# Optimization experiments

Measured on AMD Instinct MI355X. Metric: run time of the kernel, lower is better.

The kernel has to match this reference:

```python
import jax, jax.numpy as jnp
import numpy as np
import math

V, E, H, NL = 10000, 256, 512, 2
B, T = 64, 128


def _lstm_cell(x, h, c, Wih, Whh, b):
    # PyTorch gate order: i, f, g, o
    gates = x @ Wih.T + h @ Whh.T + b
    i, f, g, o = jnp.split(gates, 4, axis=-1)
    c = jax.nn.sigmoid(f) * c + jax.nn.sigmoid(i) * jnp.tanh(g)
    h = jax.nn.sigmoid(o) * jnp.tanh(c)
    return h, c


def _run_layer(xs, Wih, Whh, b):
    # xs: [T, B, D]; returns outputs [T, B, H] and final (h, c)
    Bn = xs.shape[1]
    h0 = jnp.zeros((Bn, H), xs.dtype)
    c0 = jnp.zeros((Bn, H), xs.dtype)

    def step(carry, x):
        h, c = carry
        h, c = _lstm_cell(x, h, c, Wih, Whh, b)
        return (h, c), h

    (hT, cT), ys = jax.lax.scan(step, (h0, c0), xs)
    return ys, hT, cT


def setup_inputs() -> dict:
    key = jax.random.key(0)
    ks = jax.random.split(key, 24)
    s = 0.05

    def n(k, shape):
        return jax.random.normal(k, shape, dtype=jnp.float32) * s

    inp = {
        "input_ids": jax.random.randint(ks[0], (B, T), 0, V),
        "my_attention_mask": jax.random.randint(ks[1], (B, T), 0, 2),
        "update_step": 1000,
        # encoder params
        "enc_embed": n(ks[2], (V, E)),
        "enc_Wih0": n(ks[3], (4 * H, E)),
        "enc_Whh0": n(ks[4], (4 * H, H)),
        "enc_b0": n(ks[5], (4 * H,)),
        "enc_Wih1": n(ks[6], (4 * H, H)),
        "enc_Whh1": n(ks[7], (4 * H, H)),
        "enc_b1": n(ks[8], (4 * H,)),
        # decoder params
        "dec_embed": n(ks[9], (V, E)),
        "dec_Wih0": n(ks[10], (4 * H, E)),
        "dec_Whh0": n(ks[11], (4 * H, H)),
        "dec_b0": n(ks[12], (4 * H,)),
        "dec_Wih1": n(ks[13], (4 * H, H)),
        "dec_Whh1": n(ks[14], (4 * H, H)),
        "dec_b1": n(ks[15], (4 * H,)),
        "dec_Wout": n(ks[16], (V, H)),
        "dec_bout": n(ks[17], (V,)),
    }
    return inp


def _forward(input_ids, my_attention_mask, update_step,
             enc_embed, enc_Wih0, enc_Whh0, enc_b0, enc_Wih1, enc_Whh1, enc_b1,
             dec_embed, dec_Wih0, dec_Whh0, dec_b0, dec_Wih1, dec_Whh1, dec_b1,
             dec_Wout, dec_bout):
    temp_ids = input_ids.T                      # [T, B]
    mask = my_attention_mask                    # [B, T]

    # ---- encoder: 2-layer LSTM over the full sequence ----
    emb = enc_embed[temp_ids]                   # [T, B, E]
    ys0, h0, c0 = _run_layer(emb, enc_Wih0, enc_Whh0, enc_b0)
    _, h1, c1 = _run_layer(ys0, enc_Wih1, enc_Whh1, enc_b1)

    def dec_step(carry, tok):
        dh0, dc0, dh1, dc1 = carry
        x = dec_embed[tok]                      # [B, E]
        dh0, dc0 = _lstm_cell(x, dh0, dc0, dec_Wih0, dec_Whh0, dec_b0)
        dh1, dc1 = _lstm_cell(dh0, dh1, dc1, dec_Wih1, dec_Whh1, dec_b1)
        out = dh1 @ dec_Wout.T + dec_bout       # [B, V]
        return (dh0, dc0, dh1, dc1), out

    _, dec_outs = jax.lax.scan(dec_step, (h0, c0, h1, c1), temp_ids[:-1])  # [T-1, B, V]

    # ---- mask-driven compaction: outputs[i, j] = dec_out at t where
    #      i = exclusive-cumsum of mask[j, :t]; unwritten slots stay random ----
    outputs = jax.random.uniform(jax.random.key(42), (T, B, V), dtype=jnp.float32)
    idx = jnp.cumsum(mask, axis=1) - mask       # exclusive cumsum, [B, T]
    write_i = jnp.where(mask[:, 1:] > 0, idx[:, 1:], T)   # OOB -> dropped
    vals = jnp.transpose(dec_outs, (1, 0, 2))   # [B, T-1, V]
    outputs = outputs.at[write_i, jnp.arange(B)[:, None]].set(vals, mode="drop")

    # ---- hard gumbel-softmax with straight-through ----
    temperature = max(0.5, math.exp(-0.003 * update_step))
    eps = 1e-20
    U = jax.random.uniform(jax.random.key(7), (T, B, V), dtype=jnp.float32)
    g = -jnp.log(-jnp.log(U + eps) + eps)
    y = jax.nn.softmax((outputs + g) / temperature, axis=-1)
    y_hard = jax.nn.one_hot(jnp.argmax(y, axis=-1), V, dtype=y.dtype)
    gs = jax.lax.stop_gradient(y_hard - y) + y  # [T, B, V]

    # ---- scatter back into padded layout: masked positions pull compacted
    #      gumbel onehots, unmasked positions get onehot(input id) ----
    gathered = gs[jnp.clip(idx, 0, T - 1), jnp.arange(B)[:, None]]  # [B, T, V]
    id_onehot = jax.nn.one_hot(input_ids, V, dtype=jnp.float32)     # [B, T, V]
    onehots = jnp.where((mask > 0)[:, :, None], gathered, id_onehot)
    return onehots.reshape(B * T, V)


def reference(input_ids, my_attention_mask, update_step,
              enc_embed, enc_Wih0, enc_Whh0, enc_b0, enc_Wih1, enc_Whh1, enc_b1,
              dec_embed, dec_Wih0, dec_Whh0, dec_b0, dec_Wih1, dec_Whh1, dec_b1,
              dec_Wout, dec_bout):
    return _forward(input_ids, my_attention_mask, update_step,
                    enc_embed, enc_Wih0, enc_Whh0, enc_b0, enc_Wih1, enc_Whh1, enc_b1,
                    dec_embed, dec_Wih0, dec_Whh0, dec_b0, dec_Wih1, dec_Whh1, dec_b1,
                    dec_Wout, dec_bout)
```

## Files before the change

kernel.cpp:

```cpp
#include <hip/hip_runtime.h>
#include <stdint.h>


typedef short bf16x8 __attribute__((ext_vector_type(8)));
typedef float f32x4 __attribute__((ext_vector_type(4)));

__device__ __forceinline__ void threefry2x32(uint32_t k0, uint32_t k1,
                                             uint32_t x0, uint32_t x1,
                                             uint32_t& o0, uint32_t& o1)
{
  const uint32_t k2 = k0 ^ k1 ^ 0x1BD11BDAu;
  x0 += k0; x1 += k1;
#define TF_R(r) x0 += x1; x1 = (x1 << r) | (x1 >> (32 - r)); x1 ^= x0;
  TF_R(13) TF_R(15) TF_R(26) TF_R(6)
  x0 += k1; x1 += k2 + 1u;
  TF_R(17) TF_R(29) TF_R(16) TF_R(24)
  x0 += k2; x1 += k0 + 2u;
  TF_R(13) TF_R(15) TF_R(26) TF_R(6)
  x0 += k0; x1 += k1 + 3u;
  TF_R(17) TF_R(29) TF_R(16) TF_R(24)
  x0 += k1; x1 += k2 + 4u;
  TF_R(13) TF_R(15) TF_R(26) TF_R(6)
  x0 += k2; x1 += k0 + 5u;
#undef TF_R
  o0 = x0; o1 = x1;
}

__device__ __forceinline__ float jax_uniform(uint32_t seed, uint32_t i)
{
  uint32_t o0, o1;
  threefry2x32(0u, seed, 0u, i, o0, o1);
  const uint32_t bits = o0 ^ o1;
  return __uint_as_float(0x3F800000u | (bits >> 9)) - 1.0f;
}

__device__ __forceinline__ ushort f2bf(float x)
{
  const uint32_t u = __float_as_uint(x);
  const uint32_t r = u + 0x7FFFu + ((u >> 16) & 1u);
  return (ushort)(r >> 16);
}
__device__ __forceinline__ float bf2f(ushort b)
{
  return __uint_as_float(((uint32_t)b) << 16);
}

__device__ __forceinline__ unsigned long long packkey(float f, int n)
{
  uint32_t u = __float_as_uint(f);
  u = (u & 0x80000000u) ? ~u : (u | 0x80000000u);
  return ((unsigned long long)u << 32) | (uint32_t)(0x7FFFFFFF - n);
}

__global__ __launch_bounds__(256)
void split_kernel(const float* __restrict__ src, ushort* __restrict__ hi,
                  ushort* __restrict__ lo, int n)
{
  const int i = blockIdx.x * 256 + threadIdx.x;
  if (i < n) {
    const float v = src[i];
    const ushort h = f2bf(v);
    hi[i] = h;
    lo[i] = f2bf(v - bf2f(h));
  }
}

__global__ __launch_bounds__(256)
void transpose_split_kernel(const float* __restrict__ seq,
                            ushort* __restrict__ Thi, ushort* __restrict__ Tlo)
{
  __shared__ float tile[128][65];
  const int t = blockIdx.x >> 2;
  const int kc = blockIdx.x & 3;
  const int tid = threadIdx.x;
  const float* sbase = seq + (size_t)t * 32768 + (size_t)kc * 128 * 64;
#pragma unroll
  for (int it = 0; it < 32; ++it) {
    const int idx = it * 256 + tid;
    tile[idx >> 6][idx & 63] = sbase[idx];
  }
  __syncthreads();
#pragma unroll
  for (int it = 0; it < 32; ++it) {
    const int idx = it * 256 + tid;
    const int b = idx >> 7, k = idx & 127;
    const float v = tile[k][b];
    const size_t o = ((size_t)t * 64 + b) * 512 + kc * 128 + k;
    const ushort h = f2bf(v);
    Thi[o] = h;
    Tlo[o] = f2bf(v - bf2f(h));
  }
}

template <int GATHER, int FUSED>
__global__ __launch_bounds__(256)
void gemm_split(const ushort* __restrict__ Ahi, const ushort* __restrict__ Alo,
                const int* __restrict__ ids,
                const ushort* __restrict__ Whi, const ushort* __restrict__ Wlo,
                const float* __restrict__ bias, float* __restrict__ Xg,
                const int* __restrict__ mask, const int* __restrict__ idxmap,
                unsigned long long* __restrict__ keys,
                int M, int N, int K)
{
  const int tid = threadIdx.x;
  const int wid = tid >> 6, lane = tid & 63;
  const int lm = lane & 15, quad = lane >> 4;
  const int m0 = blockIdx.x * 128 + (wid >> 1) * 64;
  const int n0 = blockIdx.y * 128 + (wid & 1) * 64;
  const int koff = quad * 8;

  size_t offA[4];
#pragma unroll
  for (int mi = 0; mi < 4; ++mi) {
    int m = m0 + mi * 16 + lm;
    int mc = m < M ? m : (M - 1);
    if (GATHER) {
      const int tok = ids[(mc & 63) * 128 + (mc >> 6)];
      offA[mi] = (size_t)tok * K;
    } else {
      offA[mi] = (size_t)mc * K;
    }
  }
  size_t offB[4];
#pragma unroll
  for (int ni = 0; ni < 4; ++ni) {
    int n = n0 + ni * 16 + lm;
    int nc = n < N ? n : (N - 1);
    offB[ni] = (size_t)nc * K;
  }

  f32x4 acc[4][4];
#pragma unroll
  for (int mi = 0; mi < 4; ++mi)
#pragma unroll
    for (int ni = 0; ni < 4; ++ni) acc[mi][ni] = (f32x4){0.f, 0.f, 0.f, 0.f};

  for (int k0 = 0; k0 < K; k0 += 32) {
    bf16x8 ah[4], al[4];
#pragma unroll
    for (int mi = 0; mi < 4; ++mi) {
      ah[mi] = *(const bf16x8*)(Ahi + offA[mi] + k0 + koff);
      al[mi] = *(const bf16x8*)(Alo + offA[mi] + k0 + koff);
    }
#pragma unroll
    for (int ni = 0; ni < 4; ++ni) {
      const bf16x8 bh = *(const bf16x8*)(Whi + offB[ni] + k0 + koff);
      const bf16x8 bl = *(const bf16x8*)(Wlo + offB[ni] + k0 + koff);
#pragma unroll
      for (int mi = 0; mi < 4; ++mi) {
        acc[mi][ni] = __builtin_amdgcn_mfma_f32_16x16x32_bf16(ah[mi], bl, acc[mi][ni], 0, 0, 0);
        acc[mi][ni] = __builtin_amdgcn_mfma_f32_16x16x32_bf16(al[mi], bh, acc[mi][ni], 0, 0, 0);
        acc[mi][ni] = __builtin_amdgcn_mfma_f32_16x16x32_bf16(ah[mi], bh, acc[mi][ni], 0, 0, 0);
      }
    }
  }

  float bv[4];
#pragma unroll
  for (int ni = 0; ni < 4; ++ni) {
    int n = n0 + ni * 16 + lm;
    bv[ni] = bias[n < N ? n : (N - 1)];
  }

  if (FUSED == 0) {
#pragma unroll
    for (int mi = 0; mi < 4; ++mi) {
#pragma unroll
      for (int i = 0; i < 4; ++i) {
        const int m = m0 + mi * 16 + quad * 4 + i;
        if (m >= M) continue;
        const int t = m >> 6, b = m & 63;
        float* base = Xg + (size_t)t * 131072 + b;
#pragma unroll
        for (int ni = 0; ni < 4; ++ni) {
          const int n = n0 + ni * 16 + lm;
          base[(size_t)n * 64] = acc[mi][ni][i] + bv[ni];
        }
      }
    }
  } else {
#pragma unroll
    for (int mi = 0; mi < 4; ++mi) {
#pragma unroll
      for (int i = 0; i < 4; ++i) {
        const int m = m0 + mi * 16 + quad * 4 + i;
        if (m >= M) continue;
        const int j = m >> 6, b = m & 63;
        const int outrow = b * 128 + j + 1;
        if (mask[outrow] == 0) continue;
        const int r = idxmap[outrow];
        const uint32_t base7 = (uint32_t)(r * 64 + b) * 10000u;
        float best = -3.0e38f;
        int bestn = 0;
#pragma unroll
        for (int ni = 0; ni < 4; ++ni) {
          const int n = n0 + ni * 16 + lm;
          if (n < N) {
            const float u7 = jax_uniform(7u, base7 + (uint32_t)n);
            const float g = -logf(-logf(u7 + 1e-20f) + 1e-20f);
            const float z = acc[mi][ni][i] + bv[ni] + g;
            if (z > best) { best = z; bestn = n; }
          }
        }
        unsigned long long key = packkey(best, bestn);
#pragma unroll
        for (int s = 1; s < 16; s <<= 1) {
          const unsigned long long o = __shfl_xor(key, s, 64);
          if (o > key) key = o;
        }
        if (lm == 0) atomicMax(keys + outrow, key);
      }
    }
  }
}

__global__ __launch_bounds__(256)
void lstm_step_mfma(const float* __restrict__ Xg,
                    const ushort* __restrict__ hHi, const ushort* __restrict__ hLo,
                    const ushort* __restrict__ WHi, const ushort* __restrict__ WLo,
                    float* __restrict__ cstate, float* __restrict__ hout,
                    ushort* __restrict__ oHi, ushort* __restrict__ oLo)
{
  const int tid = threadIdx.x;
  const int mi = tid >> 6;
  const int lane = tid & 63;
  const int lm = lane & 15, quad = lane >> 4;
  const int u = blockIdx.x * 16 + lm;
  const int koff = quad * 8;

  const ushort* aHi = hHi + (size_t)(mi * 16 + lm) * 512 + koff;
  const ushort* aLo = hLo + (size_t)(mi * 16 + lm) * 512 + koff;
  const ushort* bH[4];
  const ushort* bL[4];
#pragma unroll
  for (int g = 0; g < 4; ++g) {
    const size_t o = (size_t)(g * 512 + u) * 512 + koff;
    bH[g] = WHi + o;
    bL[g] = WLo + o;
  }

  f32x4 acc[4];
#pragma unroll
  for (int g = 0; g < 4; ++g) acc[g] = (f32x4){0.f, 0.f, 0.f, 0.f};

#pragma unroll 4
  for (int k0 = 0; k0 < 512; k0 += 32) {
    const bf16x8 ah = *(const bf16x8*)(aHi + k0);
    const bf16x8 al = *(const bf16x8*)(aLo + k0);
#pragma unroll
    for (int g = 0; g < 4; ++g) {
      const bf16x8 bh = *(const bf16x8*)(bH[g] + k0);
      const bf16x8 bl = *(const bf16x8*)(bL[g] + k0);
      acc[g] = __builtin_amdgcn_mfma_f32_16x16x32_bf16(ah, bl, acc[g], 0, 0, 0);
      acc[g] = __builtin_amdgcn_mfma_f32_16x16x32_bf16(al, bh, acc[g], 0, 0, 0);
      acc[g] = __builtin_amdgcn_mfma_f32_16x16x32_bf16(ah, bh, acc[g], 0, 0, 0);
    }
  }

  const int b0 = mi * 16 + quad * 4;
  const float4 xi = *(const float4*)(Xg + (size_t)(0 * 512 + u) * 64 + b0);
  const float4 xf = *(const float4*)(Xg + (size_t)(1 * 512 + u) * 64 + b0);
  const float4 xg = *(const float4*)(Xg + (size_t)(2 * 512 + u) * 64 + b0);
  const float4 xo = *(const float4*)(Xg + (size_t)(3 * 512 + u) * 64 + b0);
  float4 c4 = *(float4*)(cstate + (size_t)u * 64 + b0);

  float4 h4;
#pragma unroll
  for (int r = 0; r < 4; ++r) {
    const float zi = acc[0][r] + ((const float*)&xi)[r];
    const float zf = acc[1][r] + ((const float*)&xf)[r];
    const float zg = acc[2][r] + ((const float*)&xg)[r];
    const float zo = acc[3][r] + ((const float*)&xo)[r];
    const float I = 1.0f / (1.0f + expf(-zi));
    const float F = 1.0f / (1.0f + expf(-zf));
    const float G = tanhf(zg);
    const float O = 1.0f / (1.0f + expf(-zo));
    const float cn = F * ((float*)&c4)[r] + I * G;
    ((float*)&c4)[r] = cn;
    ((float*)&h4)[r] = O * tanhf(cn);
  }
  *(float4*)(cstate + (size_t)u * 64 + b0) = c4;
  *(float4*)(hout + (size_t)u * 64 + b0) = h4;
#pragma unroll
  for (int r = 0; r < 4; ++r) {
    const float hv = ((const float*)&h4)[r];
    const ushort hh = f2bf(hv);
    oHi[(size_t)(b0 + r) * 512 + u] = hh;
    oLo[(size_t)(b0 + r) * 512 + u] = f2bf(hv - bf2f(hh));
  }
}

__global__ void maskscan_kernel(const int* __restrict__ mask,
                                int* __restrict__ idxmap)
{
  const int b = threadIdx.x;
  int run = 0;
  for (int t = 0; t < 128; ++t) {
    idxmap[b * 128 + t] = run;
    run += mask[b * 128 + t];
  }
}

__global__ __launch_bounds__(256)
void t0_kernel(const int* __restrict__ mask, unsigned long long* __restrict__ keys)
{
  const int b = blockIdx.x;
  const int row = b * 128;
  if (mask[row] == 0) return;
  const int tid = threadIdx.x;
  const uint32_t base = (uint32_t)b * 10000u;
  float best = -3.0e38f;
  int bestn = 0;
  for (int v = tid; v < 10000; v += 256) {
    const float u42 = jax_uniform(42u, base + (uint32_t)v);
    const float u7 = jax_uniform(7u, base + (uint32_t)v);
    const float g = -logf(-logf(u7 + 1e-20f) + 1e-20f);
    const float z = u42 + g;
    if (z > best) { best = z; bestn = v; }
  }
  __shared__ unsigned long long sk[256];
  sk[tid] = packkey(best, bestn);
  __syncthreads();
  for (int s = 128; s > 0; s >>= 1) {
    if (tid < s) { if (sk[tid + s] > sk[tid]) sk[tid] = sk[tid + s]; }
    __syncthreads();
  }
  if (tid == 0) keys[row] = sk[0];
}

__global__ __launch_bounds__(256)
void finalize_kernel(const unsigned long long* __restrict__ keys,
                     const int* __restrict__ mask,
                     const int* __restrict__ input_ids,
                     int* __restrict__ tokens)
{
  const int row = blockIdx.x * 256 + threadIdx.x;
  if (row < 8192) {
    tokens[row] = mask[row] ? (int)(0x7FFFFFFFu - (uint32_t)(keys[row] & 0xFFFFFFFFu))
                            : input_ids[row];
  }
}

__global__ __launch_bounds__(256)
void onehot_kernel(const int* __restrict__ tokens, float* __restrict__ out)
{
  const int row = blockIdx.x;
  const int tok = tokens[row];
  float4* orow = (float4*)(out + (size_t)row * 10000);
  for (int q = threadIdx.x; q < 2500; q += 256) {
    float4 v = make_float4(0.f, 0.f, 0.f, 0.f);
    const int v0 = q << 2;
    const unsigned d = (unsigned)(tok - v0);
    if (d < 4u) ((float*)&v)[d] = 1.0f;
    orow[q] = v;
  }
}

__global__ __launch_bounds__(256)
void zero_kernel(float* __restrict__ p, int n)
{
  const int i = blockIdx.x * 256 + threadIdx.x;
  if (i < n) p[i] = 0.f;
}

extern "C" void kernel_launch(void* const* d_in, const int* in_sizes, int n_in,
                              void* d_out, int out_size, void* d_ws, size_t ws_size,
                              hipStream_t stream)
{
  const int*   input_ids = (const int*)d_in[0];
  const int*   mask      = (const int*)d_in[1];
  const float* enc_embed = (const float*)d_in[3];
  const float* enc_Wih0  = (const float*)d_in[4];
  const float* enc_Whh0  = (const float*)d_in[5];
  const float* enc_b0    = (const float*)d_in[6];
  const float* enc_Wih1  = (const float*)d_in[7];
  const float* enc_Whh1  = (const float*)d_in[8];
  const float* enc_b1    = (const float*)d_in[9];
  const float* dec_embed = (const float*)d_in[10];
  const float* dec_Wih0  = (const float*)d_in[11];
  const float* dec_Whh0  = (const float*)d_in[12];
  const float* dec_b0    = (const float*)d_in[13];
  const float* dec_Wih1  = (const float*)d_in[14];
  const float* dec_Whh1  = (const float*)d_in[15];
  const float* dec_b1    = (const float*)d_in[16];
  const float* dec_Wout  = (const float*)d_in[17];
  const float* dec_bout  = (const float*)d_in[18];

  char* O = (char*)d_out;
  float*  Xg    = (float*)(O + 0);
  ushort* sThi  = (ushort*)(O + 67108864);
  ushort* sTlo  = (ushort*)(O + 75497472);
  ushort* eEh   = (ushort*)(O + 83886080);
  ushort* eEl   = (ushort*)(O + 89006080);
  ushort* dEh   = (ushort*)(O + 94126080);
  ushort* dEl   = (ushort*)(O + 99246080);
  ushort* eW0h  = (ushort*)(O + 104366080);
  ushort* eW0l  = (ushort*)(O + 105414656);
  ushort* eW1h  = (ushort*)(O + 106463232);
  ushort* eW1l  = (ushort*)(O + 108560384);
  ushort* dW0h  = (ushort*)(O + 110657536);
  ushort* dW0l  = (ushort*)(O + 111706112);
  ushort* dW1h  = (ushort*)(O + 112754688);
  ushort* dW1l  = (ushort*)(O + 114851840);
  ushort* Woh   = (ushort*)(O + 116948992);
  ushort* Wol   = (ushort*)(O + 127188992);
  unsigned long long* keys = (unsigned long long*)(O + 137428992);
  int*    idxmap = (int*)(O + 137494528);
  ushort* eH0h = (ushort*)(O + 137527296);
  ushort* eH0l = (ushort*)(O + 139624448);
  ushort* eH1h = (ushort*)(O + 141721600);
  ushort* eH1l = (ushort*)(O + 143818752);
  ushort* dH0h = (ushort*)(O + 145915904);
  ushort* dH0l = (ushort*)(O + 148013056);
  ushort* dH1h = (ushort*)(O + 150110208);
  ushort* dH1l = (ushort*)(O + 152207360);
  ushort* hsAhi = (ushort*)(O + 154304512);
  ushort* hsAlo = (ushort*)(O + 154370048);
  ushort* hsBhi = (ushort*)(O + 154435584);
  ushort* hsBlo = (ushort*)(O + 154501120);
  ushort* hsChi = (ushort*)(O + 154566656);
  ushort* hsClo = (ushort*)(O + 154632192);
  ushort* hsDhi = (ushort*)(O + 154697728);
  ushort* hsDlo = (ushort*)(O + 154763264);

  float* seqA = (float*)d_ws;
  float* zbuf = seqA + (size_t)128 * 32768;
  float* cA   = zbuf + 32768;
  float* cB   = cA + 32768;
  float* hp0  = cB + 32768;
  float* hp1  = hp0 + 32768;
  int* tokens = (int*)(hp1 + 32768);

  zero_kernel<<<256, 256, 0, stream>>>(cA, 2 * 32768);
  zero_kernel<<<512, 256, 0, stream>>>((float*)hsAhi, 131072);
  zero_kernel<<<64, 256, 0, stream>>>((float*)keys, 16384);
  maskscan_kernel<<<1, 64, 0, stream>>>(mask, idxmap);

  split_kernel<<<10000, 256, 0, stream>>>(enc_embed, eEh, eEl, 2560000);
  split_kernel<<<10000, 256, 0, stream>>>(dec_embed, dEh, dEl, 2560000);
  split_kernel<<<2048, 256, 0, stream>>>(enc_Wih0, eW0h, eW0l, 524288);
  split_kernel<<<4096, 256, 0, stream>>>(enc_Wih1, eW1h, eW1l, 1048576);
  split_kernel<<<2048, 256, 0, stream>>>(dec_Wih0, dW0h, dW0l, 524288);
  split_kernel<<<4096, 256, 0, stream>>>(dec_Wih1, dW1h, dW1l, 1048576);
  split_kernel<<<20000, 256, 0, stream>>>(dec_Wout, Woh, Wol, 5120000);
  split_kernel<<<4096, 256, 0, stream>>>(enc_Whh0, eH0h, eH0l, 1048576);
  split_kernel<<<4096, 256, 0, stream>>>(enc_Whh1, eH1h, eH1l, 1048576);
  split_kernel<<<4096, 256, 0, stream>>>(dec_Whh0, dH0h, dH0l, 1048576);
  split_kernel<<<4096, 256, 0, stream>>>(dec_Whh1, dH1h, dH1l, 1048576);

  gemm_split<1, 0><<<dim3(64, 16), 256, 0, stream>>>(
      eEh, eEl, input_ids, eW0h, eW0l, enc_b0, Xg,
      nullptr, nullptr, nullptr, 8192, 2048, 256);
  for (int t = 0; t < 128; ++t) {
    const ushort* ih = (t & 1) ? hsBhi : hsAhi;
    const ushort* il = (t & 1) ? hsBlo : hsAlo;
    ushort* oh = (t & 1) ? hsAhi : hsBhi;
    ushort* ol = (t & 1) ? hsAlo : hsBlo;
    lstm_step_mfma<<<32, 256, 0, stream>>>(
        Xg + (size_t)t * 131072, ih, il, eH0h, eH0l, cA,
        seqA + (size_t)t * 32768, oh, ol);
  }

  transpose_split_kernel<<<512, 256, 0, stream>>>(seqA, sThi, sTlo);
  gemm_split<0, 0><<<dim3(64, 16), 256, 0, stream>>>(
      sThi, sTlo, nullptr, eW1h, eW1l, enc_b1, Xg,
      nullptr, nullptr, nullptr, 8192, 2048, 512);
  for (int t = 0; t < 128; ++t) {
    const ushort* ih = (t & 1) ? hsDhi : hsChi;
    const ushort* il = (t & 1) ? hsDlo : hsClo;
    ushort* oh = (t & 1) ? hsChi : hsDhi;
    ushort* ol = (t & 1) ? hsClo : hsDlo;
    lstm_step_mfma<<<32, 256, 0, stream>>>(
        Xg + (size_t)t * 131072, ih, il, eH1h, eH1l, cB, hp0, oh, ol);
  }

  gemm_split<1, 0><<<dim3(64, 16), 256, 0, stream>>>(
      dEh, dEl, input_ids, dW0h, dW0l, dec_b0, Xg,
      nullptr, nullptr, nullptr, 8128, 2048, 256);
  for (int j = 0; j < 127; ++j) {
    const ushort* ih = (j & 1) ? hsBhi : hsAhi;
    const ushort* il = (j & 1) ? hsBlo : hsAlo;
    ushort* oh = (j & 1) ? hsAhi : hsBhi;
    ushort* ol = (j & 1) ? hsAlo : hsBlo;
    lstm_step_mfma<<<32, 256, 0, stream>>>(
        Xg + (size_t)j * 131072, ih, il, dH0h, dH0l, cA,
        seqA + (size_t)j * 32768, oh, ol);
  }

  transpose_split_kernel<<<508, 256, 0, stream>>>(seqA, sThi, sTlo);
  gemm_split<0, 0><<<dim3(64, 16), 256, 0, stream>>>(
      sThi, sTlo, nullptr, dW1h, dW1l, dec_b1, Xg,
      nullptr, nullptr, nullptr, 8128, 2048, 512);
  for (int j = 0; j < 127; ++j) {
    const ushort* ih = (j & 1) ? hsDhi : hsChi;
    const ushort* il = (j & 1) ? hsDlo : hsClo;
    ushort* oh = (j & 1) ? hsChi : hsDhi;
    ushort* ol = (j & 1) ? hsClo : hsDlo;
    lstm_step_mfma<<<32, 256, 0, stream>>>(
        Xg + (size_t)j * 131072, ih, il, dH1h, dH1l, cB,
        seqA + (size_t)j * 32768, oh, ol);
  }

  transpose_split_kernel<<<508, 256, 0, stream>>>(seqA, sThi, sTlo);
  gemm_split<0, 1><<<dim3(64, 79), 256, 0, stream>>>(
      sThi, sTlo, nullptr, Woh, Wol, dec_bout, nullptr,
      mask, idxmap, keys, 8128, 10000, 512);
  t0_kernel<<<64, 256, 0, stream>>>(mask, keys);

  finalize_kernel<<<32, 256, 0, stream>>>(keys, mask, input_ids, tokens);
  onehot_kernel<<<8192, 256, 0, stream>>>(tokens, (float*)d_out);
}
```

Before: 13.05 ms.

## Fuse per-timestep LSTM launches into one cooperative kernel per layer

Replaces the 128/127 separate per-timestep LSTM step launches per layer with a single cooperative kernel that loops over timesteps and uses grid.sync with a threadfence between steps. This is meant to remove kernel launch overhead and inter-launch gaps across roughly 510 tiny launches. The encoder layer-1 output now goes to seqA instead of hp0, which is a scratch write. Cooperative launch requires all 32 blocks to be co-resident, and grid-wide barriers have their own cost.

Result: slower. 17.54 ms (+34.4%).

```diff
diff --git a/kernel.cpp b/kernel.cpp
--- a/kernel.cpp
+++ b/kernel.cpp
@@ -1,6 +1,9 @@
 #include <hip/hip_runtime.h>
+#include <hip/hip_cooperative_groups.h>
 #include <stdint.h>
 
+
+namespace cg = cooperative_groups;
 
 typedef short bf16x8 __attribute__((ext_vector_type(8)));
 typedef float f32x4 __attribute__((ext_vector_type(4)));
@@ -215,21 +218,24 @@
 }
 
 __global__ __launch_bounds__(256)
-void lstm_step_mfma(const float* __restrict__ Xg,
-                    const ushort* __restrict__ hHi, const ushort* __restrict__ hLo,
-                    const ushort* __restrict__ WHi, const ushort* __restrict__ WLo,
-                    float* __restrict__ cstate, float* __restrict__ hout,
-                    ushort* __restrict__ oHi, ushort* __restrict__ oLo)
-{
+void lstm_layer_coop(const float* __restrict__ Xg,
+                     const ushort* __restrict__ WHi, const ushort* __restrict__ WLo,
+                     float* __restrict__ cstate, float* __restrict__ seq_out,
+                     ushort* __restrict__ hXhi, ushort* __restrict__ hXlo,
+                     ushort* __restrict__ hYhi, ushort* __restrict__ hYlo,
+                     int nsteps)
+{
+  cg::grid_group grid = cg::this_grid();
+
   const int tid = threadIdx.x;
   const int mi = tid >> 6;
   const int lane = tid & 63;
   const int lm = lane & 15, quad = lane >> 4;
   const int u = blockIdx.x * 16 + lm;
   const int koff = quad * 8;
-
-  const ushort* aHi = hHi + (size_t)(mi * 16 + lm) * 512 + koff;
-  const ushort* aLo = hLo + (size_t)(mi * 16 + lm) * 512 + koff;
+  const int b0 = mi * 16 + quad * 4;
+
+  const size_t aoff = (size_t)(mi * 16 + lm) * 512 + koff;
   const ushort* bH[4];
   const ushort* bL[4];
 #pragma unroll
@@ -238,55 +244,69 @@
     bH[g] = WHi + o;
     bL[g] = WLo + o;
   }
-
-  f32x4 acc[4];
-#pragma unroll
-  for (int g = 0; g < 4; ++g) acc[g] = (f32x4){0.f, 0.f, 0.f, 0.f};
+  float* cptr = cstate + (size_t)u * 64 + b0;
+
+  for (int t = 0; t < nsteps; ++t) {
+    const ushort* iHi = (t & 1) ? hYhi : hXhi;
+    const ushort* iLo = (t & 1) ? hYlo : hXlo;
+    ushort* oHi = (t & 1) ? hXhi : hYhi;
+    ushort* oLo = (t & 1) ? hXlo : hYlo;
+
+    const ushort* aHi = iHi + aoff;
+    const ushort* aLo = iLo + aoff;
+
+    f32x4 acc[4];
+#pragma unroll
+    for (int g = 0; g < 4; ++g) acc[g] = (f32x4){0.f, 0.f, 0.f, 0.f};
 
 #pragma unroll 4
-  for (int k0 = 0; k0 < 512; k0 += 32) {
-    const bf16x8 ah = *(const bf16x8*)(aHi + k0);
-    const bf16x8 al = *(const bf16x8*)(aLo + k0);
-#pragma unroll
-    for (int g = 0; g < 4; ++g) {
-      const bf16x8 bh = *(const bf16x8*)(bH[g] + k0);
-      const bf16x8 bl = *(const bf16x8*)(bL[g] + k0);
-      acc[g] = __builtin_amdgcn_mfma_f32_16x16x32_bf16(ah, bl, acc[g], 0, 0, 0);
-      acc[g] = __builtin_amdgcn_mfma_f32_16x16x32_bf16(al, bh, acc[g], 0, 0, 0);
-      acc[g] = __builtin_amdgcn_mfma_f32_16x16x32_bf16(ah, bh, acc[g], 0, 0, 0);
-    }
-  }
-
-  const int b0 = mi * 16 + quad * 4;
-  const float4 xi = *(const float4*)(Xg + (size_t)(0 * 512 + u) * 64 + b0);
-  const float4 xf = *(const float4*)(Xg + (size_t)(1 * 512 + u) * 64 + b0);
-  const float4 xg = *(const float4*)(Xg + (size_t)(2 * 512 + u) * 64 + b0);
-  const float4 xo = *(const float4*)(Xg + (size_t)(3 * 512 + u) * 64 + b0);
-  float4 c4 = *(float4*)(cstate + (size_t)u * 64 + b0);
-
-  float4 h4;
-#pragma unroll
-  for (int r = 0; r < 4; ++r) {
-    const float zi = acc[0][r] + ((const float*)&xi)[r];
-    const float zf = acc[1][r] + ((const float*)&xf)[r];
-    const float zg = acc[2][r] + ((const float*)&xg)[r];
-    const float zo = acc[3][r] + ((const float*)&xo)[r];
-    const float I = 1.0f / (1.0f + expf(-zi));
-    const float F = 1.0f / (1.0f + expf(-zf));
-    const float G = tanhf(zg);
-    const float O = 1.0f / (1.0f + expf(-zo));
-    const float cn = F * ((float*)&c4)[r] + I * G;
-    ((float*)&c4)[r] = cn;
-    ((float*)&h4)[r] = O * tanhf(cn);
-  }
-  *(float4*)(cstate + (size_t)u * 64 + b0) = c4;
-  *(float4*)(hout + (size_t)u * 64 + b0) = h4;
-#pragma unroll
-  for (int r = 0; r < 4; ++r) {
-    const float hv = ((const float*)&h4)[r];
-    const ushort hh = f2bf(hv);
-    oHi[(size_t)(b0 + r) * 512 + u] = hh;
-    oLo[(size_t)(b0 + r) * 512 + u] = f2bf(hv - bf2f(hh));
+    for (int k0 = 0; k0 < 512; k0 += 32) {
+      const bf16x8 ah = *(const bf16x8*)(aHi + k0);
+      const bf16x8 al = *(const bf16x8*)(aLo + k0);
+#pragma unroll
+      for (int g = 0; g < 4; ++g) {
+        const bf16x8 bh = *(const bf16x8*)(bH[g] + k0);
+        const bf16x8 bl = *(const bf16x8*)(bL[g] + k0);
+        acc[g] = __builtin_amdgcn_mfma_f32_16x16x32_bf16(ah, bl, acc[g], 0, 0, 0);
+        acc[g] = __builtin_amdgcn_mfma_f32_16x16x32_bf16(al, bh, acc[g], 0, 0, 0);
+        acc[g] = __builtin_amdgcn_mfma_f32_16x16x32_bf16(ah, bh, acc[g], 0, 0, 0);
+      }
+    }
+
+    const float* Xt = Xg + (size_t)t * 131072;
+    const float4 xi = *(const float4*)(Xt + (size_t)(0 * 512 + u) * 64 + b0);
+    const float4 xf = *(const float4*)(Xt + (size_t)(1 * 512 + u) * 64 + b0);
+    const float4 xg = *(const float4*)(Xt + (size_t)(2 * 512 + u) * 64 + b0);
+    const float4 xo = *(const float4*)(Xt + (size_t)(3 * 512 + u) * 64 + b0);
+    float4 c4 = *(float4*)cptr;
+
+    float4 h4;
+#pragma unroll
+    for (int r = 0; r < 4; ++r) {
+      const float zi = acc[0][r] + ((const float*)&xi)[r];
+      const float zf = acc[1][r] + ((const float*)&xf)[r];
+      const float zg = acc[2][r] + ((const float*)&xg)[r];
+      const float zo = acc[3][r] + ((const float*)&xo)[r];
+      const float I = 1.0f / (1.0f + expf(-zi));
+      const float F = 1.0f / (1.0f + expf(-zf));
+      const float G = tanhf(zg);
+      const float O = 1.0f / (1.0f + expf(-zo));
+      const float cn = F * ((float*)&c4)[r] + I * G;
+      ((float*)&c4)[r] = cn;
+      ((float*)&h4)[r] = O * tanhf(cn);
+    }
+    *(float4*)cptr = c4;
+    *(float4*)(seq_out + (size_t)t * 32768 + (size_t)u * 64 + b0) = h4;
+#pragma unroll
+    for (int r = 0; r < 4; ++r) {
+      const float hv = ((const float*)&h4)[r];
+      const ushort hh = f2bf(hv);
+      oHi[(size_t)(b0 + r) * 512 + u] = hh;
+      oLo[(size_t)(b0 + r) * 512 + u] = f2bf(hv - bf2f(hh));
+    }
+
+    __threadfence();
+    grid.sync();
   }
 }
 
@@ -448,57 +468,57 @@
   split_kernel<<<4096, 256, 0, stream>>>(dec_Whh0, dH0h, dH0l, 1048576);
   split_kernel<<<4096, 256, 0, stream>>>(dec_Whh1, dH1h, dH1l, 1048576);
 
+  int nsteps128 = 128, nsteps127 = 127;
+
   gemm_split<1, 0><<<dim3(64, 16), 256, 0, stream>>>(
       eEh, eEl, input_ids, eW0h, eW0l, enc_b0, Xg,
       nullptr, nullptr, nullptr, 8192, 2048, 256);
-  for (int t = 0; t < 128; ++t) {
-    const ushort* ih = (t & 1) ? hsBhi : hsAhi;
-    const ushort* il = (t & 1) ? hsBlo : hsAlo;
-    ushort* oh = (t & 1) ? hsAhi : hsBhi;
-    ushort* ol = (t & 1) ? hsAlo : hsBlo;
-    lstm_step_mfma<<<32, 256, 0, stream>>>(
-        Xg + (size_t)t * 131072, ih, il, eH0h, eH0l, cA,
-        seqA + (size_t)t * 32768, oh, ol);
+  {
+    const float* a0 = Xg; const ushort* a1 = eH0h; const ushort* a2 = eH0l;
+    float* a3 = cA; float* a4 = seqA;
+    ushort* a5 = hsAhi; ushort* a6 = hsAlo; ushort* a7 = hsBhi; ushort* a8 = hsBlo;
+    void* args[] = {&a0, &a1, &a2, &a3, &a4, &a5, &a6, &a7, &a8, &nsteps128};
+    hipLaunchCooperativeKernel((void*)lstm_layer_coop, dim3(32), dim3(256),
+                               args, 0, stream);
   }
 
   transpose_split_kernel<<<512, 256, 0, stream>>>(seqA, sThi, sTlo);
   gemm_split<0, 0><<<dim3(64, 16), 256, 0, stream>>>(
       sThi, sTlo, nullptr, eW1h, eW1l, enc_b1, Xg,
       nullptr, nullptr, nullptr, 8192, 2048, 512);
-  for (int t = 0; t < 128; ++t) {
-    const ushort* ih = (t & 1) ? hsDhi : hsChi;
-    const ushort* il = (t & 1) ? hsDlo : hsClo;
-    ushort* oh = (t & 1) ? hsChi : hsDhi;
-    ushort* ol = (t & 1) ? hsClo : hsDlo;
-    lstm_step_mfma<<<32, 256, 0, stream>>>(
-        Xg + (size_t)t * 131072, ih, il, eH1h, eH1l, cB, hp0, oh, ol);
+  {
+    const float* a0 = Xg; const ushort* a1 = eH1h; const ushort* a2 = eH1l;
+    float* a3 = cB; float* a4 = hp0;
+    a4 = seqA;
+    ushort* a5 = hsChi; ushort* a6 = hsClo; ushort* a7 = hsDhi; ushort* a8 = hsDlo;
+    void* args[] = {&a0, &a1, &a2, &a3, &a4, &a5, &a6, &a7, &a8, &nsteps128};
+    hipLaunchCooperativeKernel((void*)lstm_layer_coop, dim3(32), dim3(256),
+                               args, 0, stream);
   }
 
   gemm_split<1, 0><<<dim3(64, 16), 256, 0, stream>>>(
       dEh, dEl, input_ids, dW0h, dW0l, dec_b0, Xg,
       nullptr, nullptr, nullptr, 8128, 2048, 256);
-  for (int j = 0; j < 127; ++j) {
-    const ushort* ih = (j & 1) ? hsBhi : hsAhi;
-    const ushort* il = (j & 1) ? hsBlo : hsAlo;
-    ushort* oh = (j & 1) ? hsAhi : hsBhi;
-    ushort* ol = (j & 1) ? hsAlo : hsBlo;
-    lstm_step_mfma<<<32, 256, 0, stream>>>(
-        Xg + (size_t)j * 131072, ih, il, dH0h, dH0l, cA,
-        seqA + (size_t)j * 32768, oh, ol);
+  {
+    const float* a0 = Xg; const ushort* a1 = dH0h; const ushort* a2 = dH0l;
+    float* a3 = cA; float* a4 = seqA;
+    ushort* a5 = hsAhi; ushort* a6 = hsAlo; ushort* a7 = hsBhi; ushort* a8 = hsBlo;
+    void* args[] = {&a0, &a1, &a2, &a3, &a4, &a5, &a6, &a7, &a8, &nsteps127};
+    hipLaunchCooperativeKernel((void*)lstm_layer_coop, dim3(32), dim3(256),
+                               args, 0, stream);
   }
 
   transpose_split_kernel<<<508, 256, 0, stream>>>(seqA, sThi, sTlo);
   gemm_split<0, 0><<<dim3(64, 16), 256, 0, stream>>>(
       sThi, sTlo, nullptr, dW1h, dW1l, dec_b1, Xg,
       nullptr, nullptr, nullptr, 8128, 2048, 512);
-  for (int j = 0; j < 127; ++j) {
-    const ushort* ih = (j & 1) ? hsDhi : hsChi;
-    const ushort* il = (j & 1) ? hsDlo : hsClo;
-    ushort* oh = (j & 1) ? hsChi : hsDhi;
-    ushort* ol = (j & 1) ? hsClo : hsDlo;
-    lstm_step_mfma<<<32, 256, 0, stream>>>(
-        Xg + (size_t)j * 131072, ih, il, dH1h, dH1l, cB,
-        seqA + (size_t)j * 32768, oh, ol);
+  {
+    const float* a0 = Xg; const ushort* a1 = dH1h; const ushort* a2 = dH1l;
+    float* a3 = cB; float* a4 = seqA;
+    ushort* a5 = hsChi; ushort* a6 = hsClo; ushort* a7 = hsDhi; ushort* a8 = hsDlo;
+    void* args[] = {&a0, &a1, &a2, &a3, &a4, &a5, &a6, &a7, &a8, &nsteps127};
+    hipLaunchCooperativeKernel((void*)lstm_layer_coop, dim3(32), dim3(256),
+                               args, 0, stream);
   }
 
   transpose_split_kernel<<<508, 256, 0, stream>>>(seqA, sThi, sTlo);
```
